# Optimization experiments

Measured on AMD Instinct MI355X. Metric: run time of the kernel, lower is better.

## Reference

```python
import jax, jax.numpy as jnp
import numpy as np

L = 8          # context_length
P = 196        # patches_per_frame
PT = 16        # patches_per_tactile_frame
N_EMBD = 768
N_HEAD = 12
BATCH = 4
T = (L + 1) + L * PT + L * P  # 1705


def build_mask(L, P, Pt):
    # image-query block rows (L*P rows)
    mi = np.zeros((L * P, L * P))
    a1 = np.zeros((L * P, L + 1))
    t1 = np.zeros((L * P, L * Pt))
    for i in range(L):
        mi[i * P:(i + 1) * P, :(i + 1) * P] = 1
        a1[i * P:(i + 2) * P, :i + 2] = 1
        t1[i * P:(i + 1) * P, :(i + 1) * Pt] = 1
    m1 = np.concatenate([a1, t1, mi], axis=1)
    # tactile-query block rows (L*Pt rows)
    a2 = np.zeros((L * Pt, L + 1))
    t2 = np.zeros((L * Pt, L * Pt))
    i2 = np.zeros((L * Pt, L * P))
    for i in range(L):
        a2[i * Pt:(i + 2) * Pt, :i + 2] = 1
        t2[i * Pt:(i + 1) * Pt, :(i + 1) * Pt] = 1
        i2[i * Pt:(i + 1) * Pt, :(i + 1) * P] = 1
    m2 = np.concatenate([a2, t2, i2], axis=1)
    # action-query rows (L+1 rows)
    a3 = np.zeros((L + 1, L + 1))
    t3 = np.zeros((L + 1, L * Pt))
    i3 = np.zeros((L + 1, L * P))
    for i in range(L + 1):
        a3[i:i + 2, :i + 2] = 1
        t3[i:i + 1, :(i + 1) * Pt] = 1
        i3[i:i + 1, :(i + 1) * P] = 1
    m3 = np.concatenate([a3, t3, i3], axis=1)
    return np.concatenate([m3, m2, m1], axis=0).astype(bool)


def setup_inputs() -> dict:
    key = jax.random.key(0)
    k1, k2, k3 = jax.random.split(key, 3)
    x = jax.random.normal(k1, (BATCH, T, N_EMBD), dtype=jnp.float32)
    W_attn = jax.random.normal(k2, (N_EMBD, 3 * N_EMBD), dtype=jnp.float32) * 0.02
    W_proj = jax.random.normal(k3, (N_EMBD, N_EMBD), dtype=jnp.float32) * 0.02
    mask = jnp.asarray(build_mask(L, P, PT))
    return {"x": x, "W_attn": W_attn, "W_proj": W_proj, "mask": mask, "n_head": N_HEAD}


def reference(x, W_attn, W_proj, mask, n_head):
    B, Tq, C = x.shape
    hd = C // n_head
    qkv = x @ W_attn                      # [B, T, 3C]
    q, k, v = jnp.split(qkv, 3, axis=-1)
    # [B, H, T, hd]
    q = q.reshape(B, Tq, n_head, hd).transpose(0, 2, 1, 3)
    k = k.reshape(B, Tq, n_head, hd).transpose(0, 2, 1, 3)
    v = v.reshape(B, Tq, n_head, hd).transpose(0, 2, 1, 3)
    scores = jnp.einsum("bhqd,bhkd->bhqk", q, k) / jnp.sqrt(jnp.float32(hd))
    scores = jnp.where(mask[None, None, :, :], scores, jnp.float32(-1e9))
    probs = jax.nn.softmax(scores, axis=-1)
    y = jnp.einsum("bhqk,bhkd->bhqd", probs, v)
    y = y.transpose(0, 2, 1, 3).reshape(B, Tq, C)
    return y @ W_proj
```

## Files before the change

kernel.cpp:

```cpp
#include <hip/hip_runtime.h>
#include <hip/hip_bf16.h>

typedef __attribute__((ext_vector_type(8))) short short8;
typedef __attribute__((ext_vector_type(4))) float f32x4;

#define MFMA16(a,b,c) __builtin_amdgcn_mfma_f32_16x16x32_bf16((a),(b),(c),0,0,0)

#define WAITVM(N) asm volatile("s_waitcnt vmcnt(" #N ")" ::: "memory")
#define BAR()     asm volatile("s_barrier" ::: "memory")

constexpr int Tt = 1705;
constexpr int Tp = 1792;
constexpr int NKT_ALL = 28;
constexpr int NH = 12, HD = 64, Bb = 4, C_ = 768;
constexpr int M_  = Bb * Tt;
constexpr int Mp  = 6912;
constexpr int NQT = 14;
constexpr int NCH = 4;
constexpr float QSCALE = 0.18033688011116016f;

static_assert(Mp % 256 == 0 && (3 * C_) % 256 == 0, "256-tile grid");

__device__ __forceinline__ void gl16(const void* g, void* l) {
  __builtin_amdgcn_global_load_lds((const __attribute__((address_space(1))) void*)g,
                                   (__attribute__((address_space(3))) void*)l, 16, 0, 0);
}

__device__ __forceinline__ float ex2(float x) {
  float r; asm("v_exp_f32 %0, %1" : "=v"(r) : "v"(x)); return r;
}

__device__ __forceinline__ int frame_of(int t) {
  return t < 9 ? t : (t < 137 ? ((t - 9) >> 4) : ((t - 137) / 196));
}

__device__ __forceinline__ int lim16(int a) {
  if (a >= Tt) return 0;
  int bnd = min(a + 15, Tt - 1);
  int fmax = (a == 0) ? 8 : frame_of(min(bnd, a < 137 ? 136 : bnd));
  return (fmax >= 8) ? Tt : 137 + (fmax + 1) * 196;
}

__global__ __launch_bounds__(256) void k_conv_x(const float* __restrict__ x,
                                                __hip_bfloat16* __restrict__ xb) {
  int i = blockIdx.x * 256 + threadIdx.x;
  if (i >= Mp * C_ / 4) return;
  float4 v = make_float4(0.f, 0.f, 0.f, 0.f);
  if (i * 4 < M_ * C_) v = ((const float4*)x)[i];
  __hip_bfloat16 o0 = __float2bfloat16(v.x), o1 = __float2bfloat16(v.y),
                 o2 = __float2bfloat16(v.z), o3 = __float2bfloat16(v.w);
  ushort4 u = make_ushort4(*(unsigned short*)&o0, *(unsigned short*)&o1,
                           *(unsigned short*)&o2, *(unsigned short*)&o3);
  ((ushort4*)xb)[i] = u;
}

__global__ __launch_bounds__(256) void k_transpose_w(const float* __restrict__ src,
                                                     __hip_bfloat16* __restrict__ dst,
                                                     int K, int N) {
  __shared__ float tile[32][33];
  int kb = blockIdx.x * 32, nb = blockIdx.y * 32;
  int tx = threadIdx.x & 31, ty = threadIdx.x >> 5;
  for (int i = 0; i < 4; i++)
    tile[ty + i * 8][tx] = src[(size_t)(kb + ty + i * 8) * N + nb + tx];
  __syncthreads();
  for (int i = 0; i < 4; i++)
    dst[(size_t)(nb + ty + i * 8) * K + kb + tx] = __float2bfloat16(tile[tx][ty + i * 8]);
}

__global__ __launch_bounds__(512) void k_gemm_qkv(const __hip_bfloat16* __restrict__ xb,
                                                  const __hip_bfloat16* __restrict__ wat,
                                                  __hip_bfloat16* __restrict__ q,
                                                  __hip_bfloat16* __restrict__ kpk,
                                                  __hip_bfloat16* __restrict__ vpk) {
  __shared__ __hip_bfloat16 As[4][256 * 32], Bs[4][256 * 32];
  const int tid = threadIdx.x;
  const int lane = tid & 63, w = tid >> 6;
  const int wr = w >> 2, wc = w & 3;
  const int l16 = lane & 15, grp = lane >> 4;
  const int m0 = blockIdx.x * 256, n0 = blockIdx.y * 256;
  constexpr int NT = C_ / 32;

  auto stage = [&](int t, int bb) {
    int k0 = t * 32;
    for (int p = 0; p < 2; p++) {
      int idx = p * 512 + tid;
      int row = idx >> 2;
      int c8 = (idx & 3) ^ ((row >> 1) & 3);
      gl16(xb  + (size_t)(m0 + row) * C_ + k0 + c8 * 8, &As[bb][idx * 8]);
      gl16(wat + (size_t)(n0 + row) * C_ + k0 + c8 * 8, &Bs[bb][idx * 8]);
    }
  };

  f32x4 acc[8][4];
  for (int i = 0; i < 8; i++)
    for (int j = 0; j < 4; j++) { f32x4 z = {0.f,0.f,0.f,0.f}; acc[i][j] = z; }

  stage(0, 0); stage(1, 1); stage(2, 2);

  for (int t = 0; t < NT; t++) {
    if (t + 3 < NT) stage(t + 3, (t + 3) & 3);
    int rem = NT - 1 - t;
    if (rem >= 3)      WAITVM(12);
    else if (rem == 2) WAITVM(8);
    else if (rem == 1) WAITVM(4);
    else               WAITVM(0);
    BAR();
    const __hip_bfloat16* Ac = As[t & 3];
    const __hip_bfloat16* Bc = Bs[t & 3];
    short8 bfr[4], afr[4];
    for (int nj = 0; nj < 4; nj++) {
      int row = wc * 64 + nj * 16 + l16;
      bfr[nj] = *(const short8*)(Bc + row * 32 + ((grp ^ ((row >> 1) & 3)) * 8));
    }
    for (int mi = 0; mi < 4; mi++) {
      int row = wr * 128 + mi * 16 + l16;
      afr[mi] = *(const short8*)(Ac + row * 32 + ((grp ^ ((row >> 1) & 3)) * 8));
    }
    __builtin_amdgcn_s_setprio(1);
    for (int mi = 0; mi < 4; mi++)
      for (int nj = 0; nj < 4; nj++)
        acc[mi][nj] = MFMA16(afr[mi], bfr[nj], acc[mi][nj]);
    __builtin_amdgcn_s_setprio(0);
    for (int mi = 0; mi < 4; mi++) {
      int row = wr * 128 + 64 + mi * 16 + l16;
      afr[mi] = *(const short8*)(Ac + row * 32 + ((grp ^ ((row >> 1) & 3)) * 8));
    }
    __builtin_amdgcn_s_setprio(1);
    for (int mi = 0; mi < 4; mi++)
      for (int nj = 0; nj < 4; nj++)
        acc[4 + mi][nj] = MFMA16(afr[mi], bfr[nj], acc[4 + mi][nj]);
    __builtin_amdgcn_s_setprio(0);
    BAR();
  }

  const int which = n0 / C_;
  const int c0 = n0 - which * C_ + wc * 64;
  for (int mi = 0; mi < 8; mi++)
    for (int r = 0; r < 4; r++) {
      int m = m0 + wr * 128 + mi * 16 + grp * 4 + r;
      if (m >= M_) continue;
      int b = m / Tt, t = m - b * Tt;
      for (int nj = 0; nj < 4; nj++) {
        int c = c0 + nj * 16 + l16;
        int h = c >> 6, d = c & 63;
        float val = acc[mi][nj][r];
        int bh = b * NH + h;
        if (which == 0) {
          q[((size_t)bh * Tp + t) * HD + d] = __float2bfloat16(val * QSCALE);
        } else if (which == 1) {
          int kt = t >> 6, jj = (t >> 4) & 3, mm = t & 15;
          int half = d >> 5, gg = (d >> 3) & 3, ss = d & 7;
          kpk[(((size_t)bh * NKT_ALL + kt) * 8 + jj * 2 + half) * 512 +
              (gg * 16 + mm) * 8 + ss] = __float2bfloat16(val);
        } else {
          int kt = t >> 6, kb2 = (t >> 5) & 1, k32 = t & 31;
          int gg = (k32 >> 2) & 3, ss = (k32 & 3) + ((k32 >> 4) & 1) * 4;
          int jt = d >> 4, mm = d & 15;
          vpk[(((size_t)bh * NKT_ALL + kt) * 8 + jt * 2 + kb2) * 512 +
              (gg * 16 + mm) * 8 + ss] = __float2bfloat16(val);
        }
      }
    }
}

__global__ __launch_bounds__(256) void k_gemm_proj64(const __hip_bfloat16* __restrict__ A,
                                                     const __hip_bfloat16* __restrict__ Bt,
                                                     float* __restrict__ out) {
  __shared__ __hip_bfloat16 As[4][64 * 32], Bs[4][128 * 32];
  const int tid = threadIdx.x;
  const int lane = tid & 63, w = tid >> 6;
  const int l16 = lane & 15, grp = lane >> 4;
  const int m0 = blockIdx.x * 64, n0 = blockIdx.y * 128;
  f32x4 acc[8];
  for (int j = 0; j < 8; j++) { f32x4 z = {0.f,0.f,0.f,0.f}; acc[j] = z; }

  auto stage = [&](int t, int bb) {
    int k0 = t * 32;
    int row = tid >> 2;
    int c8 = (tid & 3) ^ ((row >> 1) & 3);
    gl16(A + (size_t)(m0 + row) * C_ + k0 + c8 * 8, &As[bb][tid * 8]);
    for (int rr = 0; rr < 2; rr++) {
      int idx = rr * 256 + tid;
      int brow = idx >> 2;
      int bc8 = (idx & 3) ^ ((brow >> 1) & 3);
      gl16(Bt + (size_t)(n0 + brow) * C_ + k0 + bc8 * 8, &Bs[bb][idx * 8]);
    }
  };

  constexpr int NT = C_ / 32;
  stage(0, 0); stage(1, 1); stage(2, 2);

  for (int t = 0; t < NT; t++) {
    if (t + 3 < NT) stage(t + 3, (t + 3) & 3);
    int rem = NT - 1 - t;
    if (rem >= 3)      WAITVM(9);
    else if (rem == 2) WAITVM(6);
    else if (rem == 1) WAITVM(3);
    else               WAITVM(0);
    BAR();
    const __hip_bfloat16* Ac = As[t & 3];
    const __hip_bfloat16* Bc = Bs[t & 3];
    int arow = w * 16 + l16;
    short8 a = *(const short8*)(Ac + arow * 32 + ((grp ^ ((arow >> 1) & 3)) * 8));
    __builtin_amdgcn_s_setprio(1);
    for (int j = 0; j < 8; j++) {
      int brow = j * 16 + l16;
      short8 b = *(const short8*)(Bc + brow * 32 + ((grp ^ ((brow >> 1) & 3)) * 8));
      acc[j] = MFMA16(a, b, acc[j]);
    }
    __builtin_amdgcn_s_setprio(0);
    BAR();
  }

  for (int r = 0; r < 4; r++) {
    int m = m0 + w * 16 + grp * 4 + r;
    if (m >= M_) continue;
    for (int j = 0; j < 8; j++)
      out[(size_t)m * C_ + n0 + j * 16 + l16] = acc[j][r];
  }
}

union S8u { short8 v; struct { unsigned long long lo, hi; } q; unsigned u[4]; };

__device__ __forceinline__ unsigned pack2bf(float a, float b) {
  union { __hip_bfloat162 h; unsigned u; } cv;
  cv.h = __float22bfloat162_rn(make_float2(a, b));
  return cv.u;
}

__global__ __launch_bounds__(256, 2) void k_attn(const __hip_bfloat16* __restrict__ q,
                                                 const __hip_bfloat16* __restrict__ kpk,
                                                 const __hip_bfloat16* __restrict__ vpk,
                                                 __hip_bfloat16* __restrict__ Opart,
                                                 float* __restrict__ lpart) {
  const int tid = threadIdx.x, lane = tid & 63, w = tid >> 6;
  const int l16 = lane & 15, grp = lane >> 4;
  const int id = blockIdx.x;
  const int xslot = id & 7, rr_ = id >> 3;
  const int bh = xslot + 8 * (rr_ / 56);
  const int cq = rr_ % 56;
  const int qt = cq >> 2, wslot = cq & 3;
  const int ch = w;
  const int t0q = qt * 128;
  const int a0 = t0q + wslot * 32;
  const __hip_bfloat16* qb = q + (size_t)bh * Tp * HD;

  int lim[2], Cmn[2], Ath[2], Bth[2], Cth[2];
  for (int g = 0; g < 2; g++) {
    int a = a0 + g * 16;
    lim[g] = lim16(a);
    int fqmn, fql;
    if (a >= Tt) { fqmn = 8; fql = 8; }
    else {
      int bnd = min(a + 15, Tt - 1);
      fqmn = min(frame_of(a), frame_of(bnd));
      int t = a + l16;
      fql = (t >= Tt) ? 8 : frame_of(t);
    }
    Cmn[g] = min(137 + 196 * (fqmn + 1), Tt);
    Ath[g] = fql + 2;
    Bth[g] = 9 + 16 * (fql + 1);
    Cth[g] = min(137 + 196 * (fql + 1), Tt);
  }
  int limw = max(lim[0], lim[1]);
  int nktw = (limw + 63) >> 6;
  int k0t = (ch * nktw) >> 2;
  int k1t = ((ch + 1) * nktw) >> 2;

  short8 qa[2][2];
  for (int g = 0; g < 2; g++) {
    const __hip_bfloat16* qr = qb + (size_t)(a0 + g * 16 + l16) * HD + grp * 8;
    qa[g][0] = *(const short8*)(qr);
    qa[g][1] = *(const short8*)(qr + 32);
  }
  f32x4 o[2][4];
  for (int g = 0; g < 2; g++)
    for (int jt = 0; jt < 4; jt++) { f32x4 z = {0.f,0.f,0.f,0.f}; o[g][jt] = z; }
  f32x4 ps[2];
  { f32x4 z = {0.f,0.f,0.f,0.f}; ps[0] = z; ps[1] = z; }

  const short8* kbase = (const short8*)(kpk + (size_t)bh * NKT_ALL * 4096);
  const short8* vbase = (const short8*)(vpk + (size_t)bh * NKT_ALL * 4096);

  auto loadKV = [&](int kt, short8 (&kf)[4][2], short8 (&vf)[4][2]) {
    const short8* kp = kbase + (size_t)kt * 512;
    const short8* vp = vbase + (size_t)kt * 512;
    for (int j = 0; j < 4; j++)
      for (int hh = 0; hh < 2; hh++) kf[j][hh] = kp[(j * 2 + hh) * 64 + lane];
    for (int jt = 0; jt < 4; jt++)
      for (int kb2 = 0; kb2 < 2; kb2++) vf[jt][kb2] = vp[(jt * 2 + kb2) * 64 + lane];
  };

  auto do_tile = [&](int kt, const short8 (&kf)[4][2], const short8 (&vf)[4][2]) {
    const int t0k = kt * 64;
    f32x4 s[2][4];
    __builtin_amdgcn_s_setprio(1);
    for (int j = 0; j < 4; j++) {
      f32x4 z = {0.f,0.f,0.f,0.f};
      s[0][j] = MFMA16(kf[j][0], qa[0][0], z);
      s[0][j] = MFMA16(kf[j][1], qa[0][1], s[0][j]);
      s[1][j] = MFMA16(kf[j][0], qa[1][0], z);
      s[1][j] = MFMA16(kf[j][1], qa[1][1], s[1][j]);
    }
    __builtin_amdgcn_s_setprio(0);

    bool act0 = t0k < lim[0], act1 = t0k < lim[1];
    bool fullk = (t0k + 64 <= Tt);
    S8u pf[2][2];
    for (int g = 0; g < 2; g++) {
      bool act = g == 0 ? act0 : act1;
      if (!act) continue;
      bool needm = !(fullk && (t0k >= 192 ? (t0k + 64) <= Cmn[g] : Cmn[g] >= Tt));
      if (needm) {
        for (int j = 0; j < 4; j++)
          for (int r = 0; r < 4; r++) {
            int key = t0k + j * 16 + grp * 4 + r;
            int thr = key < 9 ? Ath[g] : (key < 137 ? Bth[g] : Cth[g]);
            if (key >= thr) s[g][j][r] = -1e30f;
          }
      }
      f32x4 p[4];
      for (int j = 0; j < 4; j++)
        for (int r = 0; r < 4; r++) p[j][r] = ex2(s[g][j][r]);
      ps[g] += (p[0] + p[1]) + (p[2] + p[3]);
      pf[g][0].u[0] = pack2bf(p[0][0], p[0][1]);
      pf[g][0].u[1] = pack2bf(p[0][2], p[0][3]);
      pf[g][0].u[2] = pack2bf(p[1][0], p[1][1]);
      pf[g][0].u[3] = pack2bf(p[1][2], p[1][3]);
      pf[g][1].u[0] = pack2bf(p[2][0], p[2][1]);
      pf[g][1].u[1] = pack2bf(p[2][2], p[2][3]);
      pf[g][1].u[2] = pack2bf(p[3][0], p[3][1]);
      pf[g][1].u[3] = pack2bf(p[3][2], p[3][3]);
    }

    __builtin_amdgcn_s_setprio(1);
    for (int jt = 0; jt < 4; jt++)
      for (int kb2 = 0; kb2 < 2; kb2++) {
        if (act0) o[0][jt] = MFMA16(vf[jt][kb2], pf[0][kb2].v, o[0][jt]);
        if (act1) o[1][jt] = MFMA16(vf[jt][kb2], pf[1][kb2].v, o[1][jt]);
      }
    __builtin_amdgcn_s_setprio(0);
  };

  short8 kfA[4][2], vfA[4][2], kfB[4][2], vfB[4][2];
  int kt = k0t;
  if (kt < k1t) {
    loadKV(kt, kfA, vfA);
    for (;;) {
      if (kt + 1 < k1t) loadKV(kt + 1, kfB, vfB);
      do_tile(kt, kfA, vfA);
      kt++;
      if (kt >= k1t) break;
      if (kt + 1 < k1t) loadKV(kt + 1, kfA, vfA);
      do_tile(kt, kfB, vfB);
      kt++;
      if (kt >= k1t) break;
    }
  }

  float lr[2];
  for (int g = 0; g < 2; g++) {
    float sum = (ps[g][0] + ps[g][1]) + (ps[g][2] + ps[g][3]);
    sum += __shfl_xor(sum, 16);
    sum += __shfl_xor(sum, 32);
    lr[g] = sum;
  }

  const int blk = bh * (NQT * NCH) + qt * NCH + ch;
  __hip_bfloat16* op = Opart + (size_t)blk * (128 * 64);
  for (int g = 0; g < 2; g++) {
    int row = wslot * 32 + g * 16 + l16;
    for (int jt = 0; jt < 4; jt++) {
      unsigned p01 = pack2bf(o[g][jt][0], o[g][jt][1]);
      unsigned p23 = pack2bf(o[g][jt][2], o[g][jt][3]);
      ushort4 u;
      u.x = p01 & 0xffff; u.y = p01 >> 16; u.z = p23 & 0xffff; u.w = p23 >> 16;
      *(ushort4*)(op + row * 64 + jt * 16 + grp * 4) = u;
    }
    if (grp == 0) lpart[(size_t)blk * 128 + row] = lr[g];
  }
}

__global__ __launch_bounds__(256) void k_combine(const __hip_bfloat16* __restrict__ Opart,
                                                 const float* __restrict__ lpart,
                                                 __hip_bfloat16* __restrict__ y) {
  const int tid = threadIdx.x;
  const int qt = blockIdx.x, bh = blockIdx.y;
  const int b = bh / NH, h = bh - b * NH;
  const int t0q = qt * 128;
  const int blk0 = bh * (NQT * NCH) + qt * NCH;
  __shared__ float ls[128];
  if (tid < 128) {
    float s = 0.f;
    for (int c = 0; c < NCH; c++) s += lpart[(size_t)(blk0 + c) * 128 + tid];
    ls[tid] = (s > 0.f) ? 1.0f / s : 0.f;
  }
  __syncthreads();
  for (int it = 0; it < 4; it++) {
    int e8 = it * 256 + tid;
    int e = e8 * 8;
    int row = e >> 6, d = e & 63;
    int t = t0q + row;
    if (t >= Tt) continue;
    float acc[8] = {0,0,0,0,0,0,0,0};
    for (int c = 0; c < NCH; c++) {
      short8 vv = *(const short8*)(Opart + (size_t)(blk0 + c) * (128 * 64) + e);
      for (int i = 0; i < 8; i++) {
        union { unsigned u; float f; } cv;
        cv.u = ((unsigned)(unsigned short)vv[i]) << 16;
        acc[i] += cv.f;
      }
    }
    float rinv = ls[row];
    short8 outv;
    for (int i = 0; i < 8; i += 2) {
      unsigned p = pack2bf(acc[i] * rinv, acc[i + 1] * rinv);
      outv[i] = (short)(p & 0xffff);
      outv[i + 1] = (short)(p >> 16);
    }
    *(short8*)(y + (size_t)(b * Tt + t) * C_ + h * 64 + d) = outv;
  }
}

extern "C" void kernel_launch(void* const* d_in, const int* in_sizes, int n_in,
                              void* d_out, int out_size, void* d_ws, size_t ws_size,
                              hipStream_t stream) {
  const float* x  = (const float*)d_in[0];
  const float* Wa = (const float*)d_in[1];
  const float* Wp = (const float*)d_in[2];
  float* out = (float*)d_out;

  char* ws = (char*)d_ws;
  size_t off = 0;
  auto alloc = [&](size_t bytes) { size_t r = off; off += (bytes + 255) & ~(size_t)255; return r; };
  __hip_bfloat16* xb  = (__hip_bfloat16*)(ws + alloc((size_t)Mp * C_ * 2));
  __hip_bfloat16* wat = (__hip_bfloat16*)(ws + alloc((size_t)3 * C_ * C_ * 2));
  __hip_bfloat16* wpt = (__hip_bfloat16*)(ws + alloc((size_t)C_ * C_ * 2));
  __hip_bfloat16* qb  = (__hip_bfloat16*)(ws + alloc((size_t)Bb * NH * Tp * HD * 2));
  __hip_bfloat16* kpk = (__hip_bfloat16*)(ws + alloc((size_t)Bb * NH * NKT_ALL * 4096 * 2));
  __hip_bfloat16* vpk = (__hip_bfloat16*)(ws + alloc((size_t)Bb * NH * NKT_ALL * 4096 * 2));
  __hip_bfloat16* yb  = (__hip_bfloat16*)(ws + alloc((size_t)Mp * C_ * 2));
  __hip_bfloat16* Opart = (__hip_bfloat16*)(ws + alloc((size_t)Bb * NH * NQT * NCH * 128 * 64 * 2));
  float*          lpart = (float*)(ws + alloc((size_t)Bb * NH * NQT * NCH * 128 * 4));

  k_conv_x<<<(Mp * C_ / 4 + 255) / 256, 256, 0, stream>>>(x, xb);
  k_transpose_w<<<dim3(C_ / 32, 3 * C_ / 32), 256, 0, stream>>>(Wa, wat, C_, 3 * C_);
  k_transpose_w<<<dim3(C_ / 32, C_ / 32), 256, 0, stream>>>(Wp, wpt, C_, C_);
  k_gemm_qkv<<<dim3(Mp / 256, 3 * C_ / 256), 512, 0, stream>>>(xb, wat, qb, kpk, vpk);
  k_attn<<<dim3(Bb * NH * NQT * NCH), 256, 0, stream>>>(qb, kpk, vpk, Opart, lpart);
  k_combine<<<dim3(NQT, Bb * NH), 256, 0, stream>>>(Opart, lpart, yb);
  k_gemm_proj64<<<dim3(Mp / 64, C_ / 128), 256, 0, stream>>>(yb, wpt, out);
}
```

Baseline: 232.8 us.

## Fuse prep kernels and remap attention work split across warps and blocks

```diff
diff --git a/kernel.cpp b/kernel.cpp
--- a/kernel.cpp
+++ b/kernel.cpp
@@ -41,25 +41,35 @@
   return (fmax >= 8) ? Tt : 137 + (fmax + 1) * 196;
 }
 
-__global__ __launch_bounds__(256) void k_conv_x(const float* __restrict__ x,
-                                                __hip_bfloat16* __restrict__ xb) {
-  int i = blockIdx.x * 256 + threadIdx.x;
-  if (i >= Mp * C_ / 4) return;
-  float4 v = make_float4(0.f, 0.f, 0.f, 0.f);
-  if (i * 4 < M_ * C_) v = ((const float4*)x)[i];
-  __hip_bfloat16 o0 = __float2bfloat16(v.x), o1 = __float2bfloat16(v.y),
-                 o2 = __float2bfloat16(v.z), o3 = __float2bfloat16(v.w);
-  ushort4 u = make_ushort4(*(unsigned short*)&o0, *(unsigned short*)&o1,
-                           *(unsigned short*)&o2, *(unsigned short*)&o3);
-  ((ushort4*)xb)[i] = u;
-}
-
-__global__ __launch_bounds__(256) void k_transpose_w(const float* __restrict__ src,
-                                                     __hip_bfloat16* __restrict__ dst,
-                                                     int K, int N) {
+constexpr int PREP_CONV = Mp * C_ / 4 / 256;
+constexpr int PREP_TA   = (C_ / 32) * (3 * C_ / 32);
+constexpr int PREP_TB   = (C_ / 32) * (C_ / 32);
+
+__global__ __launch_bounds__(256) void k_prep(const float* __restrict__ x,
+                                              __hip_bfloat16* __restrict__ xb,
+                                              const float* __restrict__ Wa,
+                                              __hip_bfloat16* __restrict__ wat,
+                                              const float* __restrict__ Wp,
+                                              __hip_bfloat16* __restrict__ wpt) {
   __shared__ float tile[32][33];
-  int kb = blockIdx.x * 32, nb = blockIdx.y * 32;
-  int tx = threadIdx.x & 31, ty = threadIdx.x >> 5;
+  const int bid = blockIdx.x, tid = threadIdx.x;
+  if (bid < PREP_CONV) {
+    int i = bid * 256 + tid;
+    float4 v = make_float4(0.f, 0.f, 0.f, 0.f);
+    if (i * 4 < M_ * C_) v = ((const float4*)x)[i];
+    __hip_bfloat16 o0 = __float2bfloat16(v.x), o1 = __float2bfloat16(v.y),
+                   o2 = __float2bfloat16(v.z), o3 = __float2bfloat16(v.w);
+    ushort4 u = make_ushort4(*(unsigned short*)&o0, *(unsigned short*)&o1,
+                             *(unsigned short*)&o2, *(unsigned short*)&o3);
+    ((ushort4*)xb)[i] = u;
+    return;
+  }
+  const float* src; __hip_bfloat16* dst; int N, bid2;
+  if (bid < PREP_CONV + PREP_TA) { bid2 = bid - PREP_CONV; src = Wa; dst = wat; N = 3 * C_; }
+  else                           { bid2 = bid - PREP_CONV - PREP_TA; src = Wp; dst = wpt; N = C_; }
+  const int K = C_;
+  int kb = (bid2 % (C_ / 32)) * 32, nb = (bid2 / (C_ / 32)) * 32;
+  int tx = tid & 31, ty = tid >> 5;
   for (int i = 0; i < 4; i++)
     tile[ty + i * 8][tx] = src[(size_t)(kb + ty + i * 8) * N + nb + tx];
   __syncthreads();
@@ -239,15 +249,13 @@
   const int xslot = id & 7, rr_ = id >> 3;
   const int bh = xslot + 8 * (rr_ / 56);
   const int cq = rr_ % 56;
-  const int qt = cq >> 2, wslot = cq & 3;
-  const int ch = w;
+  const int qt = cq >> 2, ch = cq & (NCH - 1);
   const int t0q = qt * 128;
-  const int a0 = t0q + wslot * 32;
   const __hip_bfloat16* qb = q + (size_t)bh * Tp * HD;
 
   int lim[2], Cmn[2], Ath[2], Bth[2], Cth[2];
   for (int g = 0; g < 2; g++) {
-    int a = a0 + g * 16;
+    int a = t0q + w * 32 + g * 16;
     lim[g] = lim16(a);
     int fqmn, fql;
     if (a >= Tt) { fqmn = 8; fql = 8; }
@@ -269,7 +277,7 @@
 
   short8 qa[2][2];
   for (int g = 0; g < 2; g++) {
-    const __hip_bfloat16* qr = qb + (size_t)(a0 + g * 16 + l16) * HD + grp * 8;
+    const __hip_bfloat16* qr = qb + (size_t)(t0q + w * 32 + g * 16 + l16) * HD + grp * 8;
     qa[g][0] = *(const short8*)(qr);
     qa[g][1] = *(const short8*)(qr + 32);
   }
@@ -294,7 +302,6 @@
   auto do_tile = [&](int kt, const short8 (&kf)[4][2], const short8 (&vf)[4][2]) {
     const int t0k = kt * 64;
     f32x4 s[2][4];
-    __builtin_amdgcn_s_setprio(1);
     for (int j = 0; j < 4; j++) {
       f32x4 z = {0.f,0.f,0.f,0.f};
       s[0][j] = MFMA16(kf[j][0], qa[0][0], z);
@@ -302,7 +309,6 @@
       s[1][j] = MFMA16(kf[j][0], qa[1][0], z);
       s[1][j] = MFMA16(kf[j][1], qa[1][1], s[1][j]);
     }
-    __builtin_amdgcn_s_setprio(0);
 
     bool act0 = t0k < lim[0], act1 = t0k < lim[1];
     bool fullk = (t0k + 64 <= Tt);
@@ -333,13 +339,11 @@
       pf[g][1].u[3] = pack2bf(p[3][2], p[3][3]);
     }
 
-    __builtin_amdgcn_s_setprio(1);
     for (int jt = 0; jt < 4; jt++)
       for (int kb2 = 0; kb2 < 2; kb2++) {
         if (act0) o[0][jt] = MFMA16(vf[jt][kb2], pf[0][kb2].v, o[0][jt]);
         if (act1) o[1][jt] = MFMA16(vf[jt][kb2], pf[1][kb2].v, o[1][jt]);
       }
-    __builtin_amdgcn_s_setprio(0);
   };
 
   short8 kfA[4][2], vfA[4][2], kfB[4][2], vfB[4][2];
@@ -366,10 +370,10 @@
     lr[g] = sum;
   }
 
-  const int blk = bh * (NQT * NCH) + qt * NCH + ch;
+  const int blk = bh * (NQT * NCH) + cq;
   __hip_bfloat16* op = Opart + (size_t)blk * (128 * 64);
   for (int g = 0; g < 2; g++) {
-    int row = wslot * 32 + g * 16 + l16;
+    int row = w * 32 + g * 16 + l16;
     for (int jt = 0; jt < 4; jt++) {
       unsigned p01 = pack2bf(o[g][jt][0], o[g][jt][1]);
       unsigned p23 = pack2bf(o[g][jt][2], o[g][jt][3]);
@@ -377,7 +381,7 @@
       u.x = p01 & 0xffff; u.y = p01 >> 16; u.z = p23 & 0xffff; u.w = p23 >> 16;
       *(ushort4*)(op + row * 64 + jt * 16 + grp * 4) = u;
     }
-    if (grp == 0) lpart[(size_t)blk * 128 + row] = lr[g];
+    if (grp == 0) lpart[(size_t)blk * 128 + w * 32 + g * 16 + l16] = lr[g];
   }
 }
 
@@ -443,9 +447,7 @@
   __hip_bfloat16* Opart = (__hip_bfloat16*)(ws + alloc((size_t)Bb * NH * NQT * NCH * 128 * 64 * 2));
   float*          lpart = (float*)(ws + alloc((size_t)Bb * NH * NQT * NCH * 128 * 4));
 
-  k_conv_x<<<(Mp * C_ / 4 + 255) / 256, 256, 0, stream>>>(x, xb);
-  k_transpose_w<<<dim3(C_ / 32, 3 * C_ / 32), 256, 0, stream>>>(Wa, wat, C_, 3 * C_);
-  k_transpose_w<<<dim3(C_ / 32, C_ / 32), 256, 0, stream>>>(Wp, wpt, C_, C_);
+  k_prep<<<PREP_CONV + PREP_TA + PREP_TB, 256, 0, stream>>>(x, xb, Wa, wat, Wp, wpt);
   k_gemm_qkv<<<dim3(Mp / 256, 3 * C_ / 256), 512, 0, stream>>>(xb, wat, qb, kpk, vpk);
   k_attn<<<dim3(Bb * NH * NQT * NCH), 256, 0, stream>>>(qb, kpk, vpk, Opart, lpart);
   k_combine<<<dim3(NQT, Bb * NH), 256, 0, stream>>>(Opart, lpart, yb);
```

After: 230.3 us. Within noise of the previous version (-1.1%).
